# Kernel optimization log

Hardware: AMD Instinct MI355X
Metric: run time of the kernel (lower is better)

## Reference

```python
import jax, jax.numpy as jnp
import numpy as np

NEG = -1.0e9  # masked_fill value from the original module

def setup_inputs() -> dict:
    key = jax.random.key(0)
    kq, kk, kv, km = jax.random.split(key, 4)
    B, H, S, D = 4, 16, 2048, 64
    Q = jax.random.normal(kq, (B, H, S, D), dtype=jnp.float32)
    K = jax.random.normal(kk, (B, H, S, D), dtype=jnp.float32)
    V = jax.random.normal(kv, (B, H, S, D), dtype=jnp.float32)
    # boolean mask, True = masked out (broadcast over batch and heads)
    mask = jax.random.randint(km, (1, 1, S, S), 0, 2).astype(jnp.bool_)
    return {"Q": Q, "K": K, "V": V, "mask": mask}

def reference(Q, K, V, mask):
    d_k = K.shape[-1]
    scale = 1.0 / jnp.sqrt(jnp.asarray(d_k, dtype=Q.dtype))
    # [B,H,S,S] attention scores
    scores = jnp.einsum("bhqd,bhkd->bhqk", Q, K) * scale
    scores = jnp.where(mask, jnp.asarray(NEG, dtype=scores.dtype), scores)
    weights = jax.nn.softmax(scores, axis=-1)
    # dropout is identity in eval mode (self.training == False)
    return jnp.einsum("bhqk,bhkd->bhqd", weights, V)
```

## Files before the change

### kernel.cpp

```cpp
#include <hip/hip_runtime.h>
#include <stdint.h>

#define SQ 2048
#define DH 64
#define NTILES (SQ / 64)

typedef __attribute__((ext_vector_type(8))) short bf16x8;
typedef __attribute__((ext_vector_type(4))) short bf16x4;
typedef __attribute__((ext_vector_type(4))) float f32x4;

static __device__ __forceinline__ unsigned short f2bf_rne(float x) {
  union { float f; uint32_t u; } v; v.f = x;
  uint32_t u = v.u;
  return (unsigned short)((u + 0x7FFFu + ((u >> 16) & 1u)) >> 16);
}

static __device__ __forceinline__ uint32_t pack_hi(float a, float b) {
  uint32_t au = __float_as_uint(a), bu = __float_as_uint(b);
#if __has_builtin(__builtin_amdgcn_perm)
  return __builtin_amdgcn_perm(bu, au, 0x07060302u);
#else
  return (bu & 0xFFFF0000u) | (au >> 16);
#endif
}

static __device__ __forceinline__ float fast_exp2(float x) {
#if __has_builtin(__builtin_amdgcn_exp2f)
  return __builtin_amdgcn_exp2f(x);
#else
  return exp2f(x);
#endif
}

#if __has_builtin(__builtin_amdgcn_mfma_f32_16x16x16_bf16)
#define MFMA_PV(a, b, c) __builtin_amdgcn_mfma_f32_16x16x16_bf16((a), (b), (c), 0, 0, 0)
#else
#define MFMA_PV(a, b, c) __builtin_amdgcn_mfma_f32_16x16x16bf16_1k((a), (b), (c), 0, 0, 0)
#endif

__global__ void pack_mask_kernel(const int* __restrict__ mask,
                                 unsigned long long* __restrict__ bits) {
  int w = blockIdx.x * 4 + (threadIdx.x >> 6);
  int lane = threadIdx.x & 63;
  int v = mask[(size_t)w * 64 + lane];
  unsigned long long b = __ballot(v != 0);
  if (lane == 0) bits[(size_t)(w & 31) * SQ + (w >> 5)] = b;
}

__global__ __launch_bounds__(256) void attn_kernel(
    const float* __restrict__ Qg, const float* __restrict__ Kg,
    const float* __restrict__ Vg, const unsigned long long* __restrict__ mbits,
    const int* __restrict__ mraw, float* __restrict__ Og) {
  __shared__ __align__(16) unsigned short Klds[64][72];
  __shared__ uint32_t Vtlds[64][35];

  const int id = blockIdx.x;
  const int bh = ((id & 7) << 3) | ((id >> 3) & 7);
  const int qblk = id >> 6;
  const int t = threadIdx.x;
  const int wave = t >> 6;
  const int lane = t & 63;
  const int col = lane & 15;
  const int quad = lane >> 4;

  const float* Qb = Qg + (size_t)bh * SQ * DH;
  const float* Kb = Kg + (size_t)bh * SQ * DH;
  const float* Vb = Vg + (size_t)bh * SQ * DH;
  float* Ob = Og + (size_t)bh * SQ * DH;

  const int q0 = qblk * 128 + wave * 32;

  const float QSCALE = 0.18033688011112042f;
  bf16x8 qf[2][2];
#pragma unroll
  for (int s = 0; s < 2; ++s) {
    int q = q0 + s * 16 + col;
#pragma unroll
    for (int j = 0; j < 2; ++j) {
      const float4* p = (const float4*)(Qb + (size_t)q * DH + j * 32 + quad * 8);
      float4 a = p[0], b = p[1];
      bf16x8 f;
      f[0] = (short)f2bf_rne(a.x * QSCALE); f[1] = (short)f2bf_rne(a.y * QSCALE);
      f[2] = (short)f2bf_rne(a.z * QSCALE); f[3] = (short)f2bf_rne(a.w * QSCALE);
      f[4] = (short)f2bf_rne(b.x * QSCALE); f[5] = (short)f2bf_rne(b.y * QSCALE);
      f[6] = (short)f2bf_rne(b.z * QSCALE); f[7] = (short)f2bf_rne(b.w * QSCALE);
      qf[s][j] = f;
    }
  }

  f32x4 acc[2][4];
#pragma unroll
  for (int s = 0; s < 2; ++s)
#pragma unroll
    for (int dt = 0; dt < 4; ++dt)
#pragma unroll
      for (int r = 0; r < 4; ++r) acc[s][dt][r] = 0.0f;
  float lsum[2] = {0.0f, 0.0f};

  for (int tile = 0; tile < NTILES; ++tile) {
    const int kk0 = tile * 64;

    unsigned long long w64[2];
    if (mbits) {
#pragma unroll
      for (int s = 0; s < 2; ++s)
        w64[s] = mbits[(size_t)tile * SQ + (q0 + s * 16 + col)];
    } else {
#pragma unroll
      for (int s = 0; s < 2; ++s) {
        int q = q0 + s * 16 + col;
        unsigned long long m = 0;
#pragma unroll
        for (int j = 0; j < 4; ++j) {
          int4 mi = *(const int4*)(mraw + (size_t)q * SQ + kk0 + j * 16 + quad * 4);
          unsigned long long nib = (unsigned long long)((mi.x != 0) | ((mi.y != 0) << 1) |
                                                        ((mi.z != 0) << 2) | ((mi.w != 0) << 3));
          m |= nib << (j * 16 + quad * 4);
        }
        w64[s] = m;
      }
    }

    __syncthreads();
#pragma unroll
    for (int i = 0; i < 4; ++i) {
      int kk = i * 16 + (t >> 4);
      int d = (t & 15) * 4;
      float4 kv = *(const float4*)(Kb + (size_t)(kk0 + kk) * DH + d);
      uint2 w;
      w.x = pack_hi(kv.x, kv.y);
      w.y = pack_hi(kv.z, kv.w);
      *(uint2*)&Klds[kk][d] = w;
    }
#pragma unroll
    for (int i = 0; i < 2; ++i) {
      int kp = i * 16 + (t >> 4);
      int d = (t & 15) * 4;
      const float* va = Vb + (size_t)(kk0 + kp * 2) * DH + d;
      float4 a = *(const float4*)va;
      float4 b = *(const float4*)(va + DH);
      Vtlds[d + 0][kp] = pack_hi(a.x, b.x);
      Vtlds[d + 1][kp] = pack_hi(a.y, b.y);
      Vtlds[d + 2][kp] = pack_hi(a.z, b.z);
      Vtlds[d + 3][kp] = pack_hi(a.w, b.w);
    }
    __syncthreads();

    uint32_t pfw[2][4][2];
#pragma unroll
    for (int kt = 0; kt < 4; ++kt) {
      const bf16x8 kf0 = *(const bf16x8*)&Klds[kt * 16 + col][quad * 8];
      const bf16x8 kf1 = *(const bf16x8*)&Klds[kt * 16 + col][32 + quad * 8];
#pragma unroll
      for (int s = 0; s < 2; ++s) {
        f32x4 st;
        st[0] = 0.f; st[1] = 0.f; st[2] = 0.f; st[3] = 0.f;
        st = __builtin_amdgcn_mfma_f32_16x16x32_bf16(kf0, qf[s][0], st, 0, 0, 0);
        st = __builtin_amdgcn_mfma_f32_16x16x32_bf16(kf1, qf[s][1], st, 0, 0, 0);
        uint32_t nib = (uint32_t)(w64[s] >> (kt * 16 + quad * 4)) & 0xFu;
        float p[4];
#pragma unroll
        for (int r = 0; r < 4; ++r) {
          float v = ((nib >> r) & 1u) ? -1.0e9f : st[r];
          float e = fast_exp2(v);
          p[r] = e;
          lsum[s] += __uint_as_float(__float_as_uint(e) & 0xFFFF0000u);
        }
        pfw[s][kt][0] = pack_hi(p[0], p[1]);
        pfw[s][kt][1] = pack_hi(p[2], p[3]);
      }
    }

#pragma unroll
    for (int kt = 0; kt < 4; ++kt) {
#pragma unroll
      for (int dt = 0; dt < 4; ++dt) {
        int drow = dt * 16 + col;
        union { uint32_t u[2]; bf16x4 v; } cv;
        cv.u[0] = Vtlds[drow][kt * 8 + quad * 2];
        cv.u[1] = Vtlds[drow][kt * 8 + quad * 2 + 1];
        union { uint32_t u[2]; bf16x4 v; } p0, p1;
        p0.u[0] = pfw[0][kt][0]; p0.u[1] = pfw[0][kt][1];
        p1.u[0] = pfw[1][kt][0]; p1.u[1] = pfw[1][kt][1];
        acc[0][dt] = MFMA_PV(cv.v, p0.v, acc[0][dt]);
        acc[1][dt] = MFMA_PV(cv.v, p1.v, acc[1][dt]);
      }
    }
  }

#pragma unroll
  for (int s = 0; s < 2; ++s) {
    float l = lsum[s];
    l += __shfl_xor(l, 16, 64);
    l += __shfl_xor(l, 32, 64);
    float inv = 1.0f / l;
    int q = q0 + s * 16 + col;
    float* orow = Ob + (size_t)q * DH;
#pragma unroll
    for (int dt = 0; dt < 4; ++dt) {
      float4 o;
      o.x = acc[s][dt][0] * inv;
      o.y = acc[s][dt][1] * inv;
      o.z = acc[s][dt][2] * inv;
      o.w = acc[s][dt][3] * inv;
      *(float4*)(orow + dt * 16 + quad * 4) = o;
    }
  }
}

extern "C" void kernel_launch(void* const* d_in, const int* in_sizes, int n_in,
                              void* d_out, int out_size, void* d_ws, size_t ws_size,
                              hipStream_t stream) {
  const float* Q = (const float*)d_in[0];
  const float* K = (const float*)d_in[1];
  const float* V = (const float*)d_in[2];
  const int* mask = (const int*)d_in[3];
  float* out = (float*)d_out;

  unsigned long long* bits = nullptr;
  const size_t need = (size_t)SQ * SQ / 8;
  if (ws_size >= need) {
    bits = (unsigned long long*)d_ws;
    pack_mask_kernel<<<(SQ * SQ / 64) / 4, 256, 0, stream>>>(mask, bits);
  }
  attn_kernel<<<1024, 256, 0, stream>>>(Q, K, V, bits, mask, out);
}
```

Measured before the change: 272.5 us.

## Double-buffer K/V tiles, widen blocks to 512 threads, compute row sums via MFMA

K/V tiles are now double-buffered in LDS: the next tile's global loads and mask bits are issued before the current tile's QK^T/softmax work and written to the alternate buffer afterward, so each iteration needs one barrier instead of two. Blocks grow to 8 waves covering 256 query rows, launched as 512 blocks, with a simpler bh mapping. The per-element scalar row-sum accumulation and cross-lane shuffles are replaced by an extra MFMA against a vector of ones. The mask-pack kernel becomes a grid-stride loop. The cost is more LDS and register pressure per block and extra MFMA issue per tile.

```diff
diff --git a/kernel.cpp b/kernel.cpp
--- a/kernel.cpp
+++ b/kernel.cpp
@@ -40,22 +40,25 @@
 
 __global__ void pack_mask_kernel(const int* __restrict__ mask,
                                  unsigned long long* __restrict__ bits) {
-  int w = blockIdx.x * 4 + (threadIdx.x >> 6);
-  int lane = threadIdx.x & 63;
-  int v = mask[(size_t)w * 64 + lane];
-  unsigned long long b = __ballot(v != 0);
-  if (lane == 0) bits[(size_t)(w & 31) * SQ + (w >> 5)] = b;
-}
-
-__global__ __launch_bounds__(256) void attn_kernel(
+  const int lane = threadIdx.x & 63;
+  const int gw = (blockIdx.x * blockDim.x + threadIdx.x) >> 6;
+  const int nw = (gridDim.x * blockDim.x) >> 6;
+  for (int w = gw; w < SQ * SQ / 64; w += nw) {
+    int v = mask[(size_t)w * 64 + lane];
+    unsigned long long b = __ballot(v != 0);
+    if (lane == 0) bits[(size_t)(w & 31) * SQ + (w >> 5)] = b;
+  }
+}
+
+__global__ __launch_bounds__(512, 4) void attn_kernel(
     const float* __restrict__ Qg, const float* __restrict__ Kg,
     const float* __restrict__ Vg, const unsigned long long* __restrict__ mbits,
     const int* __restrict__ mraw, float* __restrict__ Og) {
-  __shared__ __align__(16) unsigned short Klds[64][72];
-  __shared__ uint32_t Vtlds[64][35];
+  __shared__ __align__(16) unsigned short Klds[2][64][72];
+  __shared__ __align__(16) uint32_t Vtlds[2][64][36];
 
   const int id = blockIdx.x;
-  const int bh = ((id & 7) << 3) | ((id >> 3) & 7);
+  const int bh = id & 63;
   const int qblk = id >> 6;
   const int t = threadIdx.x;
   const int wave = t >> 6;
@@ -68,7 +71,12 @@
   const float* Vb = Vg + (size_t)bh * SQ * DH;
   float* Ob = Og + (size_t)bh * SQ * DH;
 
-  const int q0 = qblk * 128 + wave * 32;
+  const int q0 = qblk * 256 + wave * 32;
+
+  const int skk = t >> 3;
+  const int sd8 = (t & 7) * 8;
+  const int skp = t >> 4;
+  const int sd4 = (t & 15) * 4;
 
   const float QSCALE = 0.18033688011112042f;
   bf16x8 qf[2][2];
@@ -89,99 +97,116 @@
   }
 
   f32x4 acc[2][4];
-#pragma unroll
-  for (int s = 0; s < 2; ++s)
+  f32x4 accl[2];
+#pragma unroll
+  for (int s = 0; s < 2; ++s) {
 #pragma unroll
     for (int dt = 0; dt < 4; ++dt)
 #pragma unroll
       for (int r = 0; r < 4; ++r) acc[s][dt][r] = 0.0f;
-  float lsum[2] = {0.0f, 0.0f};
-
-  for (int tile = 0; tile < NTILES; ++tile) {
-    const int kk0 = tile * 64;
-
-    unsigned long long w64[2];
+#pragma unroll
+    for (int r = 0; r < 4; ++r) accl[s][r] = 0.0f;
+  }
+  bf16x4 vones;
+  vones[0] = (short)0x3F80; vones[1] = (short)0x3F80;
+  vones[2] = (short)0x3F80; vones[3] = (short)0x3F80;
+  const f32x4 fz = {0.0f, 0.0f, 0.0f, 0.0f};
+
+  auto load_mask = [&](int ti, unsigned long long m[2]) {
     if (mbits) {
 #pragma unroll
       for (int s = 0; s < 2; ++s)
-        w64[s] = mbits[(size_t)tile * SQ + (q0 + s * 16 + col)];
+        m[s] = mbits[(size_t)ti * SQ + (q0 + s * 16 + col)];
     } else {
 #pragma unroll
       for (int s = 0; s < 2; ++s) {
         int q = q0 + s * 16 + col;
-        unsigned long long m = 0;
+        unsigned long long mm = 0;
 #pragma unroll
         for (int j = 0; j < 4; ++j) {
-          int4 mi = *(const int4*)(mraw + (size_t)q * SQ + kk0 + j * 16 + quad * 4);
+          int4 mi = *(const int4*)(mraw + (size_t)q * SQ + ti * 64 + j * 16 + quad * 4);
           unsigned long long nib = (unsigned long long)((mi.x != 0) | ((mi.y != 0) << 1) |
                                                         ((mi.z != 0) << 2) | ((mi.w != 0) << 3));
-          m |= nib << (j * 16 + quad * 4);
+          mm |= nib << (j * 16 + quad * 4);
         }
-        w64[s] = m;
+        m[s] = mm;
       }
     }
-
+  };
+
+  {
+    const float4* kp = (const float4*)(Kb + (size_t)skk * DH + sd8);
+    float4 k0 = kp[0], k1 = kp[1];
+    const float* va = Vb + (size_t)(skp * 2) * DH + sd4;
+    float4 v0 = *(const float4*)va, v1 = *(const float4*)(va + DH);
+    uint4 kw;
+    kw.x = pack_hi(k0.x, k0.y); kw.y = pack_hi(k0.z, k0.w);
+    kw.z = pack_hi(k1.x, k1.y); kw.w = pack_hi(k1.z, k1.w);
+    *(uint4*)&Klds[0][skk][sd8] = kw;
+    Vtlds[0][sd4 + 0][skp] = pack_hi(v0.x, v1.x);
+    Vtlds[0][sd4 + 1][skp] = pack_hi(v0.y, v1.y);
+    Vtlds[0][sd4 + 2][skp] = pack_hi(v0.z, v1.z);
+    Vtlds[0][sd4 + 3][skp] = pack_hi(v0.w, v1.w);
+  }
+  unsigned long long mcur[2];
+  load_mask(0, mcur);
+
+  for (int tile = 0; tile < NTILES; ++tile) {
     __syncthreads();
-#pragma unroll
-    for (int i = 0; i < 4; ++i) {
-      int kk = i * 16 + (t >> 4);
-      int d = (t & 15) * 4;
-      float4 kv = *(const float4*)(Kb + (size_t)(kk0 + kk) * DH + d);
-      uint2 w;
-      w.x = pack_hi(kv.x, kv.y);
-      w.y = pack_hi(kv.z, kv.w);
-      *(uint2*)&Klds[kk][d] = w;
-    }
-#pragma unroll
-    for (int i = 0; i < 2; ++i) {
-      int kp = i * 16 + (t >> 4);
-      int d = (t & 15) * 4;
-      const float* va = Vb + (size_t)(kk0 + kp * 2) * DH + d;
-      float4 a = *(const float4*)va;
-      float4 b = *(const float4*)(va + DH);
-      Vtlds[d + 0][kp] = pack_hi(a.x, b.x);
-      Vtlds[d + 1][kp] = pack_hi(a.y, b.y);
-      Vtlds[d + 2][kp] = pack_hi(a.z, b.z);
-      Vtlds[d + 3][kp] = pack_hi(a.w, b.w);
-    }
-    __syncthreads();
+    const int cb = tile & 1, nb = cb ^ 1;
+    const int tn = (tile + 1 < NTILES) ? tile + 1 : tile;
+
+    const int kkn = tn * 64;
+    const float4* kp = (const float4*)(Kb + (size_t)(kkn + skk) * DH + sd8);
+    float4 k0 = kp[0], k1 = kp[1];
+    const float* va = Vb + (size_t)(kkn + skp * 2) * DH + sd4;
+    float4 v0 = *(const float4*)va;
+    float4 v1 = *(const float4*)(va + DH);
+    unsigned long long mnxt[2];
+    load_mask(tn, mnxt);
 
     uint32_t pfw[2][4][2];
 #pragma unroll
     for (int kt = 0; kt < 4; ++kt) {
-      const bf16x8 kf0 = *(const bf16x8*)&Klds[kt * 16 + col][quad * 8];
-      const bf16x8 kf1 = *(const bf16x8*)&Klds[kt * 16 + col][32 + quad * 8];
+      const bf16x8 kf0 = *(const bf16x8*)&Klds[cb][kt * 16 + col][quad * 8];
+      const bf16x8 kf1 = *(const bf16x8*)&Klds[cb][kt * 16 + col][32 + quad * 8];
 #pragma unroll
       for (int s = 0; s < 2; ++s) {
-        f32x4 st;
-        st[0] = 0.f; st[1] = 0.f; st[2] = 0.f; st[3] = 0.f;
-        st = __builtin_amdgcn_mfma_f32_16x16x32_bf16(kf0, qf[s][0], st, 0, 0, 0);
+        f32x4 st = __builtin_amdgcn_mfma_f32_16x16x32_bf16(kf0, qf[s][0], fz, 0, 0, 0);
         st = __builtin_amdgcn_mfma_f32_16x16x32_bf16(kf1, qf[s][1], st, 0, 0, 0);
-        uint32_t nib = (uint32_t)(w64[s] >> (kt * 16 + quad * 4)) & 0xFu;
+        uint32_t nib = (uint32_t)(mcur[s] >> (kt * 16 + quad * 4)) & 0xFu;
         float p[4];
 #pragma unroll
-        for (int r = 0; r < 4; ++r) {
-          float v = ((nib >> r) & 1u) ? -1.0e9f : st[r];
-          float e = fast_exp2(v);
-          p[r] = e;
-          lsum[s] += __uint_as_float(__float_as_uint(e) & 0xFFFF0000u);
-        }
+        for (int r = 0; r < 4; ++r)
+          p[r] = fast_exp2(((nib >> r) & 1u) ? -1.0e9f : st[r]);
         pfw[s][kt][0] = pack_hi(p[0], p[1]);
         pfw[s][kt][1] = pack_hi(p[2], p[3]);
       }
     }
 
+    {
+      uint4 kw;
+      kw.x = pack_hi(k0.x, k0.y); kw.y = pack_hi(k0.z, k0.w);
+      kw.z = pack_hi(k1.x, k1.y); kw.w = pack_hi(k1.z, k1.w);
+      *(uint4*)&Klds[nb][skk][sd8] = kw;
+      Vtlds[nb][sd4 + 0][skp] = pack_hi(v0.x, v1.x);
+      Vtlds[nb][sd4 + 1][skp] = pack_hi(v0.y, v1.y);
+      Vtlds[nb][sd4 + 2][skp] = pack_hi(v0.z, v1.z);
+      Vtlds[nb][sd4 + 3][skp] = pack_hi(v0.w, v1.w);
+    }
+    mcur[0] = mnxt[0]; mcur[1] = mnxt[1];
+
 #pragma unroll
     for (int kt = 0; kt < 4; ++kt) {
+      union { uint32_t u[2]; bf16x4 v; } p0, p1;
+      p0.u[0] = pfw[0][kt][0]; p0.u[1] = pfw[0][kt][1];
+      p1.u[0] = pfw[1][kt][0]; p1.u[1] = pfw[1][kt][1];
+      accl[0] = MFMA_PV(vones, p0.v, accl[0]);
+      accl[1] = MFMA_PV(vones, p1.v, accl[1]);
 #pragma unroll
       for (int dt = 0; dt < 4; ++dt) {
-        int drow = dt * 16 + col;
-        union { uint32_t u[2]; bf16x4 v; } cv;
-        cv.u[0] = Vtlds[drow][kt * 8 + quad * 2];
-        cv.u[1] = Vtlds[drow][kt * 8 + quad * 2 + 1];
-        union { uint32_t u[2]; bf16x4 v; } p0, p1;
-        p0.u[0] = pfw[0][kt][0]; p0.u[1] = pfw[0][kt][1];
-        p1.u[0] = pfw[1][kt][0]; p1.u[1] = pfw[1][kt][1];
+        union { uint2 u2; bf16x4 v; } cv;
+        cv.u2 = *(const uint2*)&Vtlds[cb][dt * 16 + col][kt * 8 + quad * 2];
         acc[0][dt] = MFMA_PV(cv.v, p0.v, acc[0][dt]);
         acc[1][dt] = MFMA_PV(cv.v, p1.v, acc[1][dt]);
       }
@@ -190,10 +215,7 @@
 
 #pragma unroll
   for (int s = 0; s < 2; ++s) {
-    float l = lsum[s];
-    l += __shfl_xor(l, 16, 64);
-    l += __shfl_xor(l, 32, 64);
-    float inv = 1.0f / l;
+    float inv = 1.0f / accl[s][0];
     int q = q0 + s * 16 + col;
     float* orow = Ob + (size_t)q * DH;
 #pragma unroll
@@ -221,7 +243,7 @@
   const size_t need = (size_t)SQ * SQ / 8;
   if (ws_size >= need) {
     bits = (unsigned long long*)d_ws;
-    pack_mask_kernel<<<(SQ * SQ / 64) / 4, 256, 0, stream>>>(mask, bits);
-  }
-  attn_kernel<<<1024, 256, 0, stream>>>(Q, K, V, bits, mask, out);
-}
+    pack_mask_kernel<<<1024, 256, 0, stream>>>(mask, bits);
+  }
+  attn_kernel<<<512, 512, 0, stream>>>(Q, K, V, bits, mask, out);
+}
```

New measurement: 249.6 us. 1.09x faster.
